# Kernel optimization log

Measured on AMD Instinct MI355X. Metric: run time of the kernel, lower is better.

Reference implementation:

```python
import jax, jax.numpy as jnp
import numpy as np

HIDDEN = 2048
N_HEADS = 16
N_KV_HEADS = 4
HEAD_DIM = 128
N_REP = N_HEADS // N_KV_HEADS
BATCH = 2
SEQ = 2048
SCALE = HEAD_DIM ** -0.5
NEG = -1e9


def apply_rope(x, freqs):
    # x: (b, s, h, d); freqs: (s, d//2) angles. Interleaved-pair rotation.
    cos = jnp.cos(freqs)[None, :, None, :]
    sin = jnp.sin(freqs)[None, :, None, :]
    x1 = x[..., 0::2]
    x2 = x[..., 1::2]
    r1 = x1 * cos - x2 * sin
    r2 = x1 * sin + x2 * cos
    return jnp.stack([r1, r2], axis=-1).reshape(x.shape)


def setup_inputs() -> dict:
    key = jax.random.key(0)
    ks = jax.random.split(key, 6)
    x = jax.random.normal(ks[0], (BATCH, SEQ, HIDDEN), dtype=jnp.float32)
    wq = jax.random.normal(ks[1], (N_HEADS * HEAD_DIM, HIDDEN), dtype=jnp.float32) * 0.02
    wk = jax.random.normal(ks[2], (N_KV_HEADS * HEAD_DIM, HIDDEN), dtype=jnp.float32) * 0.02
    wv = jax.random.normal(ks[3], (N_KV_HEADS * HEAD_DIM, HIDDEN), dtype=jnp.float32) * 0.02
    wo = jax.random.normal(ks[4], (HIDDEN, N_HEADS * HEAD_DIM), dtype=jnp.float32) * 0.02
    # RoPE angle table: pos * theta^{-2i/d}
    inv_freq = 1.0 / (10000.0 ** (jnp.arange(0, HEAD_DIM, 2, dtype=jnp.float32) / HEAD_DIM))
    rope_freqs = jnp.arange(SEQ, dtype=jnp.float32)[:, None] * inv_freq[None, :]  # (S, d/2)
    # additive causal mask
    causal = jnp.tril(jnp.ones((SEQ, SEQ), dtype=bool))
    mask = jnp.where(causal, 0.0, NEG).astype(jnp.float32)[None, None]  # (1,1,S,S)
    return {"x": x, "wq": wq, "wk": wk, "wv": wv, "wo": wo,
            "rope_freqs": rope_freqs, "mask": mask}


def reference(x, wq, wk, wv, wo, rope_freqs, mask):
    b, s, _ = x.shape
    q = (x @ wq.T).reshape(b, s, N_HEADS, HEAD_DIM)
    k = (x @ wk.T).reshape(b, s, N_KV_HEADS, HEAD_DIM)
    v = (x @ wv.T).reshape(b, s, N_KV_HEADS, HEAD_DIM)
    q = apply_rope(q, rope_freqs)
    k = apply_rope(k, rope_freqs)
    new_k, new_v = k, v  # kv cache (no prior cache, start_pos=0)
    # GQA: repeat each kv head n_rep times (matches expand+reshape in source)
    k_rep = jnp.repeat(k, N_REP, axis=2)  # (b, s, n_heads, d)
    v_rep = jnp.repeat(v, N_REP, axis=2)
    scores = jnp.einsum('bqhd,bkhd->bhqk', q, k_rep) * SCALE
    scores = scores + mask
    attn = jax.nn.softmax(scores.astype(jnp.float32), axis=-1).astype(q.dtype)
    out = jnp.einsum('bhqk,bkhd->bqhd', attn, v_rep).reshape(b, s, -1)
    return out @ wo.T, (new_k, new_v)
```

## Files before the change

### kernel.cpp

```cpp
#include <hip/hip_runtime.h>
#include <hip/hip_bf16.h>

#define NH 16
#define NKV 4
#define HD 128
#define QSCALE 0.1275174272f

using bf16x8 = __attribute__((ext_vector_type(8))) __bf16;
using f32x4  = __attribute__((ext_vector_type(4))) float;
using u16x8  = __attribute__((ext_vector_type(8))) unsigned short;
using u16x2  = __attribute__((ext_vector_type(2))) unsigned short;

__device__ __forceinline__ unsigned short f2b(float f) {
  __hip_bfloat16 h = __float2bfloat16(f);
  return __builtin_bit_cast(unsigned short, h);
}
__device__ __forceinline__ float b2f(unsigned short u) {
  unsigned int v = ((unsigned int)u) << 16;
  return __builtin_bit_cast(float, v);
}

__device__ __forceinline__ void glds16(const unsigned short* g, unsigned short* l) {
  __builtin_amdgcn_global_load_lds(
      (const __attribute__((address_space(1))) unsigned int*)(const void*)g,
      (__attribute__((address_space(3))) unsigned int*)(void*)l, 16, 0, 0);
}

__global__ __launch_bounds__(256) void cvt_fused(const float* __restrict__ x,
                                                 const float* __restrict__ wq,
                                                 const float* __restrict__ wk,
                                                 const float* __restrict__ wv,
                                                 const float* __restrict__ wo,
                                                 unsigned short* __restrict__ xb,
                                                 unsigned short* __restrict__ wqkvb,
                                                 unsigned short* __restrict__ wob) {
  int i = blockIdx.x * 256 + threadIdx.x;
  const float* src;
  unsigned short* dst;
  int off;
  if (i < 1048576)      { src = x;  dst = xb;              off = i; }
  else if (i < 1572864) { src = wq; dst = wqkvb;           off = i - 1048576; }
  else if (i < 1703936) { src = wk; dst = wqkvb + 4194304; off = i - 1572864; }
  else if (i < 1835008) { src = wv; dst = wqkvb + 5242880; off = i - 1703936; }
  else                  { src = wo; dst = wob;             off = i - 1835008; }
  const float4* s4 = reinterpret_cast<const float4*>(src) + (size_t)off * 2;
  float4 v0 = s4[0], v1 = s4[1];
  u16x8 o;
  o[0] = f2b(v0.x); o[1] = f2b(v0.y); o[2] = f2b(v0.z); o[3] = f2b(v0.w);
  o[4] = f2b(v1.x); o[5] = f2b(v1.y); o[6] = f2b(v1.z); o[7] = f2b(v1.w);
  reinterpret_cast<u16x8*>(dst)[off] = o;
}

template<int CF32>
__global__ __launch_bounds__(512, 1) void gemm8(const unsigned short* __restrict__ A,
                                                const unsigned short* __restrict__ B,
                                                void* __restrict__ C,
                                                int N, int K, int nbx) {
  __shared__ unsigned short As[3][128 * 64];
  __shared__ unsigned short Bs[3][256 * 64];
  const int tid = threadIdx.x, lane = tid & 63;
  const int wid = tid >> 6, wm = wid >> 2, wn = wid & 3;
  const int cpx = gridDim.x >> 3;
  const int wgid = (blockIdx.x & 7) * cpx + (blockIdx.x >> 3);
  const int bx = wgid % nbx, by = wgid / nbx;
  const int row0 = by * 128, col0 = bx * 256;
  const int fr = lane & 15, g = lane >> 4;
  const int NT = K >> 6;

  size_t offA[2], offB[4];
#pragma unroll
  for (int l = 0; l < 2; l++) {
    int cid = tid + l * 512, R = cid >> 3, phys = cid & 7, cl = phys ^ (R & 7);
    offA[l] = (size_t)(row0 + R) * K + cl * 8;
  }
#pragma unroll
  for (int l = 0; l < 4; l++) {
    int cid = tid + l * 512, R = cid >> 3, phys = cid & 7, cl = phys ^ (R & 7);
    offB[l] = (size_t)(col0 + R) * K + cl * 8;
  }

  auto stage0 = [&](int t, int sb) {
    int k0 = t * 64;
    glds16(A + offA[0] + k0, &As[sb][tid * 8]);
    glds16(A + offA[1] + k0, &As[sb][(tid + 512) * 8]);
    glds16(B + offB[0] + k0, &Bs[sb][tid * 8]);
  };
  auto stage1 = [&](int t, int sb) {
    int k0 = t * 64;
    glds16(B + offB[1] + k0, &Bs[sb][(tid + 512) * 8]);
    glds16(B + offB[2] + k0, &Bs[sb][(tid + 1024) * 8]);
    glds16(B + offB[3] + k0, &Bs[sb][(tid + 1536) * 8]);
  };

  const int ca = fr & 7;
  auto ldA = [&](int rb, int mf, int ks) {
    return *reinterpret_cast<const bf16x8*>(
        &As[rb][(wm * 64 + mf * 16 + fr) * 64 + (((ks << 2) | g) ^ ca) * 8]);
  };
  auto ldB = [&](int rb, int nf, int ks) {
    return *reinterpret_cast<const bf16x8*>(
        &Bs[rb][(wn * 64 + nf * 16 + fr) * 64 + (((ks << 2) | g) ^ ca) * 8]);
  };

  f32x4 acc[4][4];
#pragma unroll
  for (int i = 0; i < 4; i++)
#pragma unroll
    for (int j = 0; j < 4; j++) acc[i][j] = f32x4{0.f, 0.f, 0.f, 0.f};

  stage0(0, 0); stage1(0, 0);
  stage0(1, 1); stage1(1, 1);
  asm volatile("s_waitcnt vmcnt(6)" ::: "memory");
  __builtin_amdgcn_s_barrier();
  __builtin_amdgcn_sched_barrier(0);

  int rb = 0, sb = 2;
#pragma unroll 1
  for (int t = 0; t < NT; ++t) {
    bf16x8 bfr[4][2];
#pragma unroll
    for (int nf = 0; nf < 4; nf++) { bfr[nf][0] = ldB(rb, nf, 0); bfr[nf][1] = ldB(rb, nf, 1); }
    bf16x8 a0[2][2];
#pragma unroll
    for (int mf = 0; mf < 2; mf++) { a0[mf][0] = ldA(rb, mf, 0); a0[mf][1] = ldA(rb, mf, 1); }
    if (t + 2 < NT) stage0(t + 2, sb);
    __builtin_amdgcn_s_barrier();
    asm volatile("s_waitcnt lgkmcnt(0)" ::: "memory");
    __builtin_amdgcn_sched_barrier(0);
    __builtin_amdgcn_s_setprio(1);
#pragma unroll
    for (int mf = 0; mf < 2; mf++)
#pragma unroll
      for (int nf = 0; nf < 4; nf++) {
        acc[mf][nf] = __builtin_amdgcn_mfma_f32_16x16x32_bf16(a0[mf][0], bfr[nf][0], acc[mf][nf], 0, 0, 0);
        acc[mf][nf] = __builtin_amdgcn_mfma_f32_16x16x32_bf16(a0[mf][1], bfr[nf][1], acc[mf][nf], 0, 0, 0);
      }
    __builtin_amdgcn_s_setprio(0);
    __builtin_amdgcn_sched_barrier(0);
    __builtin_amdgcn_s_barrier();

    bf16x8 a1[2][2];
#pragma unroll
    for (int mf = 0; mf < 2; mf++) { a1[mf][0] = ldA(rb, mf + 2, 0); a1[mf][1] = ldA(rb, mf + 2, 1); }
    if (t + 2 < NT) stage1(t + 2, sb);
    __builtin_amdgcn_s_barrier();
    asm volatile("s_waitcnt lgkmcnt(0)" ::: "memory");
    __builtin_amdgcn_sched_barrier(0);
    __builtin_amdgcn_s_setprio(1);
#pragma unroll
    for (int mf = 0; mf < 2; mf++)
#pragma unroll
      for (int nf = 0; nf < 4; nf++) {
        acc[mf + 2][nf] = __builtin_amdgcn_mfma_f32_16x16x32_bf16(a1[mf][0], bfr[nf][0], acc[mf + 2][nf], 0, 0, 0);
        acc[mf + 2][nf] = __builtin_amdgcn_mfma_f32_16x16x32_bf16(a1[mf][1], bfr[nf][1], acc[mf + 2][nf], 0, 0, 0);
      }
    __builtin_amdgcn_s_setprio(0);
    __builtin_amdgcn_sched_barrier(0);

    if (t + 1 < NT) {
      if (t + 2 < NT) asm volatile("s_waitcnt vmcnt(6)" ::: "memory");
      else            asm volatile("s_waitcnt vmcnt(0)" ::: "memory");
      __builtin_amdgcn_s_barrier();
      __builtin_amdgcn_sched_barrier(0);
    }
    rb = rb == 2 ? 0 : rb + 1;
    sb = sb == 2 ? 0 : sb + 1;
  }

#pragma unroll
  for (int i = 0; i < 4; i++) {
#pragma unroll
    for (int j = 0; j < 4; j++) {
      int rbase = row0 + wm * 64 + i * 16 + g * 4;
      int cb = col0 + wn * 64 + j * 16 + fr;
#pragma unroll
      for (int r = 0; r < 4; r++) {
        if (CF32)
          reinterpret_cast<float*>(C)[(size_t)(rbase + r) * N + cb] = acc[i][j][r];
        else
          reinterpret_cast<unsigned short*>(C)[(size_t)(rbase + r) * N + cb] = f2b(acc[i][j][r]);
      }
    }
  }
}

__global__ __launch_bounds__(256) void rope_kernel(const unsigned short* __restrict__ qkv,
                                                   const float* __restrict__ freqs,
                                                   unsigned short* __restrict__ qro,
                                                   unsigned short* __restrict__ kro,
                                                   float* __restrict__ newk) {
  const int NQ = 4096 * 16 * 64;
  const int NK = 4096 * 4 * 64;
  int idx = blockIdx.x * 256 + threadIdx.x;
  if (idx >= NQ + NK) return;
  if (idx < NQ) {
    int i = idx & 63;
    int h = (idx >> 6) & 15;
    int row = idx >> 10;
    int s = row & 2047, b = row >> 11;
    float f = freqs[s * 64 + i];
    float c = cosf(f), sn = sinf(f);
    u16x2 xv = *reinterpret_cast<const u16x2*>(qkv + (size_t)row * 3072 + h * 128 + 2 * i);
    float x1 = b2f(xv.x), x2 = b2f(xv.y);
    float r1 = (x1 * c - x2 * sn) * QSCALE;
    float r2 = (x1 * sn + x2 * c) * QSCALE;
    u16x2 o; o.x = f2b(r1); o.y = f2b(r2);
    *reinterpret_cast<u16x2*>(qro + ((size_t)(b * 16 + h) * 2048 + s) * 128 + 2 * i) = o;
  } else {
    idx -= NQ;
    int i = idx & 63;
    int h = (idx >> 6) & 3;
    int row = idx >> 8;
    int s = row & 2047, b = row >> 11;
    float f = freqs[s * 64 + i];
    float c = cosf(f), sn = sinf(f);
    u16x2 xv = *reinterpret_cast<const u16x2*>(qkv + (size_t)row * 3072 + 2048 + h * 128 + 2 * i);
    float x1 = b2f(xv.x), x2 = b2f(xv.y);
    float r1 = x1 * c - x2 * sn;
    float r2 = x1 * sn + x2 * c;
    u16x2 o; o.x = f2b(r1); o.y = f2b(r2);
    *reinterpret_cast<u16x2*>(kro + ((size_t)(b * 4 + h) * 2048 + s) * 128 + 2 * i) = o;
    float2 of; of.x = r1; of.y = r2;
    *reinterpret_cast<float2*>(newk + (size_t)row * 512 + h * 128 + 2 * i) = of;
  }
}

__global__ __launch_bounds__(256) void vtrans_kernel(const unsigned short* __restrict__ qkv,
                                                     unsigned short* __restrict__ vt,
                                                     float* __restrict__ newv) {
  __shared__ unsigned short T[32][136];
  const int st = blockIdx.x;
  const int kvh = blockIdx.y & 3, b = blockIdx.y >> 2;
  const int s0 = st * 32;
  const int t = threadIdx.x;
  const int ls = t >> 3;
  const int ch = (t & 7) * 2;
  const unsigned short* src = qkv + (size_t)(b * 2048 + s0 + ls) * 3072 + 2560 + kvh * 128 + ch * 8;
  u16x8 a0 = *reinterpret_cast<const u16x8*>(src);
  u16x8 a1 = *reinterpret_cast<const u16x8*>(src + 8);
  *reinterpret_cast<u16x8*>(&T[ls][ch * 8])     = a0;
  *reinterpret_cast<u16x8*>(&T[ls][ch * 8 + 8]) = a1;
  float* nv = newv + (size_t)(b * 2048 + s0 + ls) * 512 + kvh * 128 + ch * 8;
  float4 f0, f1, f2, f3;
  f0.x = b2f(a0[0]); f0.y = b2f(a0[1]); f0.z = b2f(a0[2]); f0.w = b2f(a0[3]);
  f1.x = b2f(a0[4]); f1.y = b2f(a0[5]); f1.z = b2f(a0[6]); f1.w = b2f(a0[7]);
  f2.x = b2f(a1[0]); f2.y = b2f(a1[1]); f2.z = b2f(a1[2]); f2.w = b2f(a1[3]);
  f3.x = b2f(a1[4]); f3.y = b2f(a1[5]); f3.z = b2f(a1[6]); f3.w = b2f(a1[7]);
  reinterpret_cast<float4*>(nv)[0] = f0;
  reinterpret_cast<float4*>(nv)[1] = f1;
  reinterpret_cast<float4*>(nv)[2] = f2;
  reinterpret_cast<float4*>(nv)[3] = f3;
  __syncthreads();
  const int d = t >> 1, half = t & 1;
  unsigned short* dst = vt + ((size_t)(b * 4 + kvh) * 128 + d) * 2048 + s0 + half * 16;
  u16x8 o0, o1;
#pragma unroll
  for (int q = 0; q < 8; q++) {
    int slot = half * 16 + q;
    int kl = ((slot >> 2) & 1) * 16 + (slot >> 3) * 4 + (slot & 3);
    o0[q] = T[kl][d];
  }
#pragma unroll
  for (int q = 0; q < 8; q++) {
    int slot = half * 16 + 8 + q;
    int kl = ((slot >> 2) & 1) * 16 + (slot >> 3) * 4 + (slot & 3);
    o1[q] = T[kl][d];
  }
  reinterpret_cast<u16x8*>(dst)[0] = o0;
  reinterpret_cast<u16x8*>(dst)[1] = o1;
}

__global__ __launch_bounds__(256, 4) void attn_kernel(const unsigned short* __restrict__ qro,
                                                      const unsigned short* __restrict__ kro,
                                                      const unsigned short* __restrict__ vt,
                                                      unsigned short* __restrict__ out) {
  __shared__ unsigned short Ks[2][32 * 128];
  __shared__ unsigned short Vs[2][64 * 64];
  const int tid = threadIdx.x, lane = tid & 63, w = tid >> 6;
  const int kvhb = blockIdx.x & 7;
  const int kvh = kvhb & 3, b = kvhb >> 2;
  const int t = 127 - (blockIdx.x >> 3);
  const int h = kvh * 4 + w;
  const int qbase = t * 16;
  const int fr = lane & 15, g = lane >> 4, fk = g * 8;
  const unsigned short* Kp = kro + (size_t)(b * 4 + kvh) * 2048 * 128;
  const unsigned short* Vtp = vt + (size_t)(b * 4 + kvh) * 128 * 2048;
  const unsigned short* Qp = qro + ((size_t)(b * 16 + h) * 2048 + qbase) * 128;

  bf16x8 qf[4];
#pragma unroll
  for (int kk = 0; kk < 4; kk++)
    qf[kk] = *reinterpret_cast<const bf16x8*>(Qp + fr * 128 + kk * 32 + fk);

  u16x8 onesu;
#pragma unroll
  for (int j = 0; j < 8; j++) onesu[j] = 0x3F80;
  bf16x8 ones = __builtin_bit_cast(bf16x8, onesu);

  f32x4 o[8];
#pragma unroll
  for (int dt = 0; dt < 8; dt++) o[dt] = f32x4{0.f, 0.f, 0.f, 0.f};
  f32x4 dacc = f32x4{0.f, 0.f, 0.f, 0.f};
  const int qrow_s = qbase + fr;
  const int nfull = (qbase >= 31) ? ((qbase - 31) >> 5) + 1 : 0;
  const int niter = nfull + 1;

  const int krow = w * 8 + (lane >> 4);
  const int kcol = lane & 15;
  const int vrow = w * 16 + (lane >> 3);
  const int vcol = lane & 7;

  auto stage = [&](int kv0, int buf) {
    unsigned short* Kb = &Ks[buf][0];
    unsigned short* Vb = &Vs[buf][0];
#pragma unroll
    for (int j = 0; j < 2; j++) {
      int r = krow + j * 4;
      glds16(Kp + (size_t)(kv0 + r) * 128 + ((kcol ^ (r & 7)) * 8),
             Kb + (w * 8 + j * 4) * 128);
    }
#pragma unroll
    for (int j = 0; j < 2; j++) {
      int r = vrow + j * 8;
      int u = vcol ^ (r & 7);
      int d = 2 * r + (u >> 2);
      glds16(Vtp + (size_t)d * 2048 + kv0 + (u & 3) * 8,
             Vb + (w * 16 + j * 8) * 64);
    }
  };

  auto step = [&](int kv0, bool mask, int buf) {
    const unsigned short* Kb = &Ks[buf][0];
    const unsigned short* Vb = &Vs[buf][0];
    f32x4 sc[2];
    sc[0] = sc[1] = f32x4{0.f, 0.f, 0.f, 0.f};
    __builtin_amdgcn_s_setprio(1);
#pragma unroll
    for (int kk = 0; kk < 4; kk++) {
      int blk = ((kk * 4 + g) ^ (fr & 7)) * 8;
      bf16x8 ka0 = *reinterpret_cast<const bf16x8*>(Kb + (fr +  0) * 128 + blk);
      bf16x8 ka1 = *reinterpret_cast<const bf16x8*>(Kb + (fr + 16) * 128 + blk);
      sc[0] = __builtin_amdgcn_mfma_f32_16x16x32_bf16(ka0, qf[kk], sc[0], 0, 0, 0);
      sc[1] = __builtin_amdgcn_mfma_f32_16x16x32_bf16(ka1, qf[kk], sc[1], 0, 0, 0);
    }
    __builtin_amdgcn_s_setprio(0);
#pragma unroll
    for (int s = 0; s < 2; s++)
#pragma unroll
      for (int r = 0; r < 4; r++) {
        float v = sc[s][r];
        if (mask && (kv0 + 16 * s + 4 * g + r > qrow_s)) v = -1e30f;
        sc[s][r] = __builtin_amdgcn_exp2f(v);
      }
    u16x8 pau;
#pragma unroll
    for (int j = 0; j < 4; j++) {
      pau[j]     = f2b(sc[0][j]);
      pau[4 + j] = f2b(sc[1][j]);
    }
    bf16x8 pa = __builtin_bit_cast(bf16x8, pau);
    dacc = __builtin_amdgcn_mfma_f32_16x16x32_bf16(pa, ones, dacc, 0, 0, 0);
    __builtin_amdgcn_s_setprio(1);
#pragma unroll
    for (int dt = 0; dt < 8; dt++) {
      int jr = dt * 8 + (fr >> 1);
      int c = ((fr & 1) * 4 + g) ^ (fr >> 1);
      bf16x8 vf = *reinterpret_cast<const bf16x8*>(Vb + jr * 64 + c * 8);
      o[dt] = __builtin_amdgcn_mfma_f32_16x16x32_bf16(pa, vf, o[dt], 0, 0, 0);
    }
    __builtin_amdgcn_s_setprio(0);
  };

  stage(0, 0);
  int buf = 0;
  for (int i = 0; i < niter; i++) {
    __syncthreads();
    if (i + 1 < niter) stage((i + 1) * 32, buf ^ 1);
    step(i * 32, i == nfull, buf);
    buf ^= 1;
  }

#pragma unroll
  for (int r = 0; r < 4; r++) {
    float inv = 1.0f / dacc[r];
    int qrow = qbase + g * 4 + r;
    size_t rowoff = ((size_t)b * 2048 + qrow) * 2048 + (size_t)h * 128;
#pragma unroll
    for (int dt = 0; dt < 8; dt++)
      out[rowoff + dt * 16 + fr] = f2b(o[dt][r] * inv);
  }
}

extern "C" void kernel_launch(void* const* d_in, const int* in_sizes, int n_in,
                              void* d_out, int out_size, void* d_ws, size_t ws_size,
                              hipStream_t stream) {
  const float* x  = (const float*)d_in[0];
  const float* wq = (const float*)d_in[1];
  const float* wk = (const float*)d_in[2];
  const float* wv = (const float*)d_in[3];
  const float* wo = (const float*)d_in[4];
  const float* freqs = (const float*)d_in[5];

  char* ws = (char*)d_ws;
  unsigned short* xb    = (unsigned short*)(ws);
  unsigned short* attn  = xb;
  unsigned short* wqkvb = (unsigned short*)(ws + 16777216);
  unsigned short* wob   = (unsigned short*)(ws + 29360128);
  unsigned short* qkv   = (unsigned short*)(ws + 37748736);
  unsigned short* qro   = (unsigned short*)(ws + 62914560);
  unsigned short* kro   = (unsigned short*)(ws + 79691776);
  unsigned short* vt    = (unsigned short*)(ws + 83886080);

  float* out_o = (float*)d_out;
  float* out_k = (float*)d_out + 8388608;
  float* out_v = (float*)d_out + 10485760;

  cvt_fused<<<9216, 256, 0, stream>>>(x, wq, wk, wv, wo, xb, wqkvb, wob);

  gemm8<0><<<384, 512, 0, stream>>>(xb, wqkvb, qkv, 3072, 2048, 12);

  rope_kernel<<<20480, 256, 0, stream>>>(qkv, freqs, qro, kro, out_k);
  vtrans_kernel<<<dim3(64, 8), 256, 0, stream>>>(qkv, vt, out_v);

  attn_kernel<<<1024, 256, 0, stream>>>(qro, kro, vt, attn);

  gemm8<1><<<256, 512, 0, stream>>>(attn, wob, out_o, 2048, 2048, 8);
}
```

Baseline: 212.1 us.

## Enlarge GEMM block tile to 256x256 with K-step 32 and packed LDS layout

Replaces the 128x256 tile, K=64 GEMM with a 256x256 tile and a K step of 32. Each LDS line of 64 elements now holds two rows' 32-wide K slices, with a new XOR swizzle to avoid bank conflicts. Each wave now holds 8x4 accumulator fragments, doubling per-block operand reuse and halving global loads per output. In exchange the grids shrink to 192 and 128 blocks, which leaves many of the 256 CUs idle, and register pressure rises.

```diff
diff --git a/kernel.cpp b/kernel.cpp
--- a/kernel.cpp
+++ b/kernel.cpp
@@ -52,113 +52,97 @@
 }
 
 template<int CF32>
-__global__ __launch_bounds__(512, 1) void gemm8(const unsigned short* __restrict__ A,
-                                                const unsigned short* __restrict__ B,
-                                                void* __restrict__ C,
-                                                int N, int K, int nbx) {
-  __shared__ unsigned short As[3][128 * 64];
-  __shared__ unsigned short Bs[3][256 * 64];
+__global__ __launch_bounds__(512, 1) void gemm256(const unsigned short* __restrict__ A,
+                                                  const unsigned short* __restrict__ B,
+                                                  void* __restrict__ C,
+                                                  int N, int K, int nbx) {
+  __shared__ unsigned short As[3 * 8192];
+  __shared__ unsigned short Bs[3 * 8192];
   const int tid = threadIdx.x, lane = tid & 63;
   const int wid = tid >> 6, wm = wid >> 2, wn = wid & 3;
   const int cpx = gridDim.x >> 3;
   const int wgid = (blockIdx.x & 7) * cpx + (blockIdx.x >> 3);
   const int bx = wgid % nbx, by = wgid / nbx;
-  const int row0 = by * 128, col0 = bx * 256;
+  const int row0 = by * 256, col0 = bx * 256;
   const int fr = lane & 15, g = lane >> 4;
-  const int NT = K >> 6;
-
-  size_t offA[2], offB[4];
+  const int NT = K >> 5;
+
+  size_t offA[2], offB[2];
 #pragma unroll
   for (int l = 0; l < 2; l++) {
     int cid = tid + l * 512, R = cid >> 3, phys = cid & 7, cl = phys ^ (R & 7);
-    offA[l] = (size_t)(row0 + R) * K + cl * 8;
-  }
-#pragma unroll
-  for (int l = 0; l < 4; l++) {
-    int cid = tid + l * 512, R = cid >> 3, phys = cid & 7, cl = phys ^ (R & 7);
-    offB[l] = (size_t)(col0 + R) * K + cl * 8;
-  }
-
-  auto stage0 = [&](int t, int sb) {
-    int k0 = t * 64;
-    glds16(A + offA[0] + k0, &As[sb][tid * 8]);
-    glds16(A + offA[1] + k0, &As[sb][(tid + 512) * 8]);
-    glds16(B + offB[0] + k0, &Bs[sb][tid * 8]);
+    int row = 2 * R + (cl >> 2), kc = cl & 3;
+    offA[l] = (size_t)(row0 + row) * K + kc * 8;
+    offB[l] = (size_t)(col0 + row) * K + kc * 8;
+  }
+
+  auto stage_half = [&](int t, int sb, int h) {
+    int k0 = t * 32;
+    glds16(A + offA[h] + k0, &As[sb * 8192 + (tid + h * 512) * 8]);
+    glds16(B + offB[h] + k0, &Bs[sb * 8192 + (tid + h * 512) * 8]);
   };
-  auto stage1 = [&](int t, int sb) {
-    int k0 = t * 64;
-    glds16(B + offB[1] + k0, &Bs[sb][(tid + 512) * 8]);
-    glds16(B + offB[2] + k0, &Bs[sb][(tid + 1024) * 8]);
-    glds16(B + offB[3] + k0, &Bs[sb][(tid + 1536) * 8]);
+
+  auto ldfrag = [&](const unsigned short* buf, int row) {
+    int R = row >> 1;
+    int phys = ((((row & 1) << 2) | g) ^ (R & 7));
+    return *reinterpret_cast<const bf16x8*>(&buf[R * 64 + phys * 8]);
   };
 
-  const int ca = fr & 7;
-  auto ldA = [&](int rb, int mf, int ks) {
-    return *reinterpret_cast<const bf16x8*>(
-        &As[rb][(wm * 64 + mf * 16 + fr) * 64 + (((ks << 2) | g) ^ ca) * 8]);
-  };
-  auto ldB = [&](int rb, int nf, int ks) {
-    return *reinterpret_cast<const bf16x8*>(
-        &Bs[rb][(wn * 64 + nf * 16 + fr) * 64 + (((ks << 2) | g) ^ ca) * 8]);
-  };
-
-  f32x4 acc[4][4];
-#pragma unroll
-  for (int i = 0; i < 4; i++)
+  f32x4 acc[8][4];
+#pragma unroll
+  for (int i = 0; i < 8; i++)
 #pragma unroll
     for (int j = 0; j < 4; j++) acc[i][j] = f32x4{0.f, 0.f, 0.f, 0.f};
 
-  stage0(0, 0); stage1(0, 0);
-  stage0(1, 1); stage1(1, 1);
-  asm volatile("s_waitcnt vmcnt(6)" ::: "memory");
+  stage_half(0, 0, 0); stage_half(0, 0, 1);
+  stage_half(1, 1, 0); stage_half(1, 1, 1);
+  asm volatile("s_waitcnt vmcnt(4)" ::: "memory");
   __builtin_amdgcn_s_barrier();
   __builtin_amdgcn_sched_barrier(0);
 
   int rb = 0, sb = 2;
 #pragma unroll 1
   for (int t = 0; t < NT; ++t) {
-    bf16x8 bfr[4][2];
-#pragma unroll
-    for (int nf = 0; nf < 4; nf++) { bfr[nf][0] = ldB(rb, nf, 0); bfr[nf][1] = ldB(rb, nf, 1); }
-    bf16x8 a0[2][2];
-#pragma unroll
-    for (int mf = 0; mf < 2; mf++) { a0[mf][0] = ldA(rb, mf, 0); a0[mf][1] = ldA(rb, mf, 1); }
-    if (t + 2 < NT) stage0(t + 2, sb);
+    const unsigned short* Ar = &As[rb * 8192];
+    const unsigned short* Br = &Bs[rb * 8192];
+
+    bf16x8 bfr[4], a[4];
+#pragma unroll
+    for (int nf = 0; nf < 4; nf++) bfr[nf] = ldfrag(Br, wn * 64 + nf * 16 + fr);
+#pragma unroll
+    for (int mf = 0; mf < 4; mf++) a[mf] = ldfrag(Ar, wm * 128 + mf * 16 + fr);
+    if (t + 2 < NT) stage_half(t + 2, sb, 0);
     __builtin_amdgcn_s_barrier();
     asm volatile("s_waitcnt lgkmcnt(0)" ::: "memory");
     __builtin_amdgcn_sched_barrier(0);
     __builtin_amdgcn_s_setprio(1);
 #pragma unroll
-    for (int mf = 0; mf < 2; mf++)
-#pragma unroll
-      for (int nf = 0; nf < 4; nf++) {
-        acc[mf][nf] = __builtin_amdgcn_mfma_f32_16x16x32_bf16(a0[mf][0], bfr[nf][0], acc[mf][nf], 0, 0, 0);
-        acc[mf][nf] = __builtin_amdgcn_mfma_f32_16x16x32_bf16(a0[mf][1], bfr[nf][1], acc[mf][nf], 0, 0, 0);
-      }
+    for (int mf = 0; mf < 4; mf++)
+#pragma unroll
+      for (int nf = 0; nf < 4; nf++)
+        acc[mf][nf] = __builtin_amdgcn_mfma_f32_16x16x32_bf16(a[mf], bfr[nf], acc[mf][nf], 0, 0, 0);
     __builtin_amdgcn_s_setprio(0);
     __builtin_amdgcn_sched_barrier(0);
     __builtin_amdgcn_s_barrier();
 
-    bf16x8 a1[2][2];
-#pragma unroll
-    for (int mf = 0; mf < 2; mf++) { a1[mf][0] = ldA(rb, mf + 2, 0); a1[mf][1] = ldA(rb, mf + 2, 1); }
-    if (t + 2 < NT) stage1(t + 2, sb);
+    bf16x8 a2[4];
+#pragma unroll
+    for (int mf = 0; mf < 4; mf++) a2[mf] = ldfrag(Ar, wm * 128 + (mf + 4) * 16 + fr);
+    if (t + 2 < NT) stage_half(t + 2, sb, 1);
     __builtin_amdgcn_s_barrier();
     asm volatile("s_waitcnt lgkmcnt(0)" ::: "memory");
     __builtin_amdgcn_sched_barrier(0);
     __builtin_amdgcn_s_setprio(1);
 #pragma unroll
-    for (int mf = 0; mf < 2; mf++)
-#pragma unroll
-      for (int nf = 0; nf < 4; nf++) {
-        acc[mf + 2][nf] = __builtin_amdgcn_mfma_f32_16x16x32_bf16(a1[mf][0], bfr[nf][0], acc[mf + 2][nf], 0, 0, 0);
-        acc[mf + 2][nf] = __builtin_amdgcn_mfma_f32_16x16x32_bf16(a1[mf][1], bfr[nf][1], acc[mf + 2][nf], 0, 0, 0);
-      }
+    for (int mf = 0; mf < 4; mf++)
+#pragma unroll
+      for (int nf = 0; nf < 4; nf++)
+        acc[mf + 4][nf] = __builtin_amdgcn_mfma_f32_16x16x32_bf16(a2[mf], bfr[nf], acc[mf + 4][nf], 0, 0, 0);
     __builtin_amdgcn_s_setprio(0);
     __builtin_amdgcn_sched_barrier(0);
 
     if (t + 1 < NT) {
-      if (t + 2 < NT) asm volatile("s_waitcnt vmcnt(6)" ::: "memory");
+      if (t + 2 < NT) asm volatile("s_waitcnt vmcnt(4)" ::: "memory");
       else            asm volatile("s_waitcnt vmcnt(0)" ::: "memory");
       __builtin_amdgcn_s_barrier();
       __builtin_amdgcn_sched_barrier(0);
@@ -168,10 +152,10 @@
   }
 
 #pragma unroll
-  for (int i = 0; i < 4; i++) {
+  for (int i = 0; i < 8; i++) {
 #pragma unroll
     for (int j = 0; j < 4; j++) {
-      int rbase = row0 + wm * 64 + i * 16 + g * 4;
+      int rbase = row0 + wm * 128 + i * 16 + g * 4;
       int cb = col0 + wn * 64 + j * 16 + fr;
 #pragma unroll
       for (int r = 0; r < 4; r++) {
@@ -417,12 +401,12 @@
 
   cvt_fused<<<9216, 256, 0, stream>>>(x, wq, wk, wv, wo, xb, wqkvb, wob);
 
-  gemm8<0><<<384, 512, 0, stream>>>(xb, wqkvb, qkv, 3072, 2048, 12);
+  gemm256<0><<<192, 512, 0, stream>>>(xb, wqkvb, qkv, 3072, 2048, 12);
 
   rope_kernel<<<20480, 256, 0, stream>>>(qkv, freqs, qro, kro, out_k);
   vtrans_kernel<<<dim3(64, 8), 256, 0, stream>>>(qkv, vt, out_v);
 
   attn_kernel<<<1024, 256, 0, stream>>>(qro, kro, vt, attn);
 
-  gemm8<1><<<256, 512, 0, stream>>>(attn, wob, out_o, 2048, 2048, 8);
-}
+  gemm256<1><<<128, 512, 0, stream>>>(attn, wob, out_o, 2048, 2048, 8);
+}
```

Result: slower. 222.1 us (+4.7%).
